# Kernel optimization log

Hardware: AMD Instinct MI355X
Metric: run time of the kernel (lower is better)

The kernel has to match this reference:

```python
import jax, jax.numpy as jnp
import numpy as np

K = 3  # per_pix_kernel


def conv2d(x, w, b, pad):
    y = jax.lax.conv_general_dilated(
        x, w, window_strides=(1, 1), padding=[(pad, pad), (pad, pad)],
        dimension_numbers=('NCHW', 'OIHW', 'NCHW'))
    return y + b[None, :, None, None]


def per_pix_apply(x, kmap):
    # x: [B,C,H,W]; kmap: [B,K*K,H,W] (tanh-activated per-pixel kernels)
    # out[b,c,h,w] = sum_j patch_j(x)[b,c,h,w] * kmap[b,j,h,w]
    B, C, H, W = x.shape
    p = K // 2
    xp = jnp.pad(x, ((0, 0), (0, 0), (p, p), (p, p)))
    patches = jnp.stack(
        [xp[:, :, di:di + H, dj:dj + W] for di in range(K) for dj in range(K)],
        axis=1)  # [B, K*K, C, H, W]
    return jnp.einsum('bjchw,bjhw->bchw', patches, kmap)


def setup_inputs() -> dict:
    key = jax.random.key(0)
    ks = jax.random.split(key, 7)
    B, C, H, W = 4, 64, 256, 256
    kk = K * K  # 9
    s = 0.05
    return {
        'feature': jax.random.normal(ks[0], (B, C, H, W), jnp.float32),
        'w_sharp': jax.random.normal(ks[1], (kk, C, 5, 5), jnp.float32) * s,
        'b_sharp': jnp.zeros((kk,), jnp.float32),
        'w_r1': jax.random.normal(ks[2], (kk, C, 3, 3), jnp.float32) * s,
        'b_r1': jnp.zeros((kk,), jnp.float32),
        'w_r2': jax.random.normal(ks[3], (kk, kk, 3, 3), jnp.float32) * s,
        'b_r2': jnp.zeros((kk,), jnp.float32),
    }


def reference(feature, w_sharp, b_sharp, w_r1, b_r1, w_r2, b_r2):
    # sharp_attention = local_conv: 5x5 conv -> tanh -> per-pixel dynamic filter
    att_kernels = jnp.tanh(conv2d(feature, w_sharp, b_sharp, pad=2))  # [B,9,H,W]
    attention_feature = per_pix_apply(feature, att_kernels)           # [B,C,H,W]
    # reblur_filer (ratio == 1): conv3x3 -> conv3x3 -> tanh
    d = feature - attention_feature
    r = conv2d(d, w_r1, b_r1, pad=1)
    r = conv2d(r, w_r2, b_r2, pad=1)
    reblur_filter = jnp.tanh(r)  # [B,9,H,W]
    return reblur_filter, attention_feature
```

## Files before the change

kernel.cpp:

```cpp
#include <hip/hip_runtime.h>

#define B_ 4
#define C_ 64
#define H_ 256
#define W_ 256
#define KK 9

typedef __attribute__((ext_vector_type(8))) short short8;
typedef __attribute__((ext_vector_type(4))) float float4_;

static __device__ __forceinline__ unsigned short f2bf(float f) {
    unsigned int u = __builtin_bit_cast(unsigned int, f);
    unsigned int r = (u + 0x7fffu + ((u >> 16) & 1u)) >> 16;
    return (unsigned short)r;
}
static __device__ __forceinline__ float bf2f(short s) {
    return __builtin_bit_cast(float, (unsigned int)((unsigned short)s) << 16);
}

__global__ __launch_bounds__(256) void nchw2nhwc(
    const float* __restrict__ x, unsigned short* __restrict__ xh)
{
    __shared__ unsigned short t[256 * 66];
    int row = blockIdx.x;
    int b = row >> 8;
    const float* src = x + ((size_t)b * 64) * 65536 + (size_t)(row & 255) * 256;
    int tid = threadIdx.x;

    #pragma unroll 4
    for (int c = 0; c < 64; ++c)
        t[tid * 66 + c] = f2bf(src[(size_t)c * 65536 + tid]);
    __syncthreads();

    unsigned short* dst = xh + (size_t)row * 256 * 64;
    #pragma unroll
    for (int it = 0; it < 8; ++it) {
        int idx = it * 256 + tid;
        int pix = idx >> 3, g = idx & 7;
        short8 v = *(const short8*)(&t[pix * 66 + g * 8]);
        *(short8*)(dst + (size_t)pix * 64 + g * 8) = v;
    }
}

__global__ __launch_bounds__(256) void wprep_all(
    const float* __restrict__ w5, const float* __restrict__ w3,
    unsigned short* __restrict__ wb, unsigned short* __restrict__ wb3)
{
    int i = blockIdx.x * 256 + threadIdx.x;
    if (i < 25600) {
        int tap = i >> 10;
        int q = (i >> 7) & 7;
        int n = (i >> 3) & 15;
        int e = i & 7;
        int c = q * 8 + e;
        int di = tap / 5, dj = tap % 5;
        float v = (n < KK) ? w5[((n * C_ + c) * 5 + di) * 5 + dj] : 0.f;
        wb[i] = f2bf(v);
    } else if (i < 34816) {
        int k = i - 25600;
        int tap = k >> 10;
        int q = (k >> 7) & 7;
        int n = (k >> 3) & 15;
        int e = k & 7;
        int c = q * 8 + e;
        int di = tap / 3, dj = tap % 3;
        float v = (n < KK) ? w3[((n * C_ + c) * 3 + di) * 3 + dj] : 0.f;
        wb3[k] = f2bf(v);
    }
}

__global__ __launch_bounds__(256) void conv5_mfma(
    const unsigned short* __restrict__ xh,
    const unsigned short* __restrict__ wb,
    const float* __restrict__ bias,
    unsigned short* __restrict__ att)
{
    __shared__ unsigned short xs[20 * 20 * 64];

    int tid = threadIdx.x;
    int bx = blockIdx.x & 15;
    int by = (blockIdx.x >> 4) & 15;
    int b  = blockIdx.x >> 8;
    int h0 = by * 16, w0 = bx * 16;

    for (int q = tid; q < 400 * 8; q += 256) {
        int p = q & 7;
        int pix = q >> 3;
        int py = pix / 20, px = pix % 20;
        int gy = h0 + py - 2, gx = w0 + px - 2;
        short8 v = (short8)0;
        if (gy >= 0 && gy < H_ && gx >= 0 && gx < W_)
            v = *(const short8*)(xh + ((size_t)((b * 256 + gy) * 256 + gx) * 64 + p * 8));
        *(short8*)(&xs[(pix << 6) + ((p ^ (pix & 7)) << 3)]) = v;
    }
    __syncthreads();

    int lane = tid & 63;
    int wid  = tid >> 6;
    int m16  = lane & 15;
    int lq   = lane >> 4;

    float4_ acc[4];
    float bj = (m16 < KK) ? bias[m16] : 0.f;
    #pragma unroll
    for (int r = 0; r < 4; ++r) acc[r] = (float4_){bj, bj, bj, bj};

    #pragma unroll
    for (int dj = 0; dj < 5; ++dj) {
        short8 bfr[5][2];
        #pragma unroll
        for (int di = 0; di < 5; ++di) {
            int tap = di * 5 + dj;
            bfr[di][0] = *(const short8*)(wb + (((tap * 8 + lq) * 16 + m16) * 8));
            bfr[di][1] = *(const short8*)(wb + (((tap * 8 + 4 + lq) * 16 + m16) * 8));
        }
        int px = m16 + dj;
        #pragma unroll
        for (int s = 0; s < 8; ++s) {
            int pix = (wid * 4 + s) * 20 + px;
            int c0 = lq ^ (pix & 7);
            short8 a0 = *(const short8*)(&xs[(pix << 6) + (c0 << 3)]);
            short8 a1 = *(const short8*)(&xs[(pix << 6) + ((c0 ^ 4) << 3)]);
            #pragma unroll
            for (int di = 0; di < 5; ++di) {
                int r = s - di;
                if (r < 0 || r > 3) continue;
                acc[r] = __builtin_amdgcn_mfma_f32_16x16x32_bf16(a0, bfr[di][0], acc[r], 0, 0, 0);
                acc[r] = __builtin_amdgcn_mfma_f32_16x16x32_bf16(a1, bfr[di][1], acc[r], 0, 0, 0);
            }
        }
    }

    if (m16 < KK) {
        #pragma unroll
        for (int r = 0; r < 4; ++r) {
            int py = h0 + wid * 4 + r;
            #pragma unroll
            for (int reg = 0; reg < 4; ++reg) {
                int px = w0 + lq * 4 + reg;
                att[((b * KK + m16) << 16) | (py << 8) | px] = f2bf(tanhf(acc[r][reg]));
            }
        }
    }
}

__global__ __launch_bounds__(256) void perpix_nhwc(
    const unsigned short* __restrict__ xh, const unsigned short* __restrict__ att,
    float* __restrict__ attf, unsigned short* __restrict__ dh)
{
    int t = blockIdx.x * 256 + threadIdx.x;
    int g = t & 7;
    int pix = t >> 3;
    int b = pix >> 16;
    int hw = pix & 65535;
    int h = hw >> 8, w = hw & 255;

    float a[KK];
    #pragma unroll
    for (int j = 0; j < KK; ++j)
        a[j] = bf2f(att[((b * KK + j) << 16) | hw]);

    float s[8] = {0, 0, 0, 0, 0, 0, 0, 0};
    float xc[8] = {0, 0, 0, 0, 0, 0, 0, 0};
    #pragma unroll
    for (int di = 0; di < 3; ++di) {
        int y = h + di - 1;
        #pragma unroll
        for (int dj = 0; dj < 3; ++dj) {
            int xq = w + dj - 1;
            if (y < 0 || y >= H_ || xq < 0 || xq >= W_) continue;
            short8 v = *(const short8*)(xh + ((size_t)((b << 16) | (y << 8) | xq) * 64 + g * 8));
            float aj = a[di * 3 + dj];
            #pragma unroll
            for (int i = 0; i < 8; ++i) {
                float xv = bf2f(v[i]);
                s[i] += xv * aj;
                if (di == 1 && dj == 1) xc[i] = xv;
            }
        }
    }

    #pragma unroll
    for (int i = 0; i < 8; ++i)
        attf[((size_t)(b * C_ + g * 8 + i) << 16) | hw] = s[i];

    short8 dv;
    #pragma unroll
    for (int i = 0; i < 8; ++i) dv[i] = (short)f2bf(xc[i] - s[i]);
    *(short8*)(dh + (size_t)pix * 64 + g * 8) = dv;
}

__global__ __launch_bounds__(256) void conv3_mfma(
    const unsigned short* __restrict__ dh,
    const unsigned short* __restrict__ wb3,
    const float* __restrict__ bias,
    unsigned short* __restrict__ r1h)
{
    __shared__ unsigned short xs[18 * 18 * 64];

    int tid = threadIdx.x;
    int bx = blockIdx.x & 15;
    int by = (blockIdx.x >> 4) & 15;
    int b  = blockIdx.x >> 8;
    int h0 = by * 16, w0 = bx * 16;

    for (int q = tid; q < 324 * 8; q += 256) {
        int p = q & 7;
        int pix = q >> 3;
        int py = pix / 18, px = pix % 18;
        int gy = h0 + py - 1, gx = w0 + px - 1;
        short8 v = (short8)0;
        if (gy >= 0 && gy < H_ && gx >= 0 && gx < W_)
            v = *(const short8*)(dh + ((size_t)((b * 256 + gy) * 256 + gx) * 64 + p * 8));
        *(short8*)(&xs[(pix << 6) + ((p ^ (pix & 7)) << 3)]) = v;
    }
    __syncthreads();

    int lane = tid & 63;
    int wid  = tid >> 6;
    int m16  = lane & 15;
    int lq   = lane >> 4;

    float4_ acc[4];
    float bj = (m16 < KK) ? bias[m16] : 0.f;
    #pragma unroll
    for (int r = 0; r < 4; ++r) acc[r] = (float4_){bj, bj, bj, bj};

    #pragma unroll
    for (int dj = 0; dj < 3; ++dj) {
        short8 bfr[3][2];
        #pragma unroll
        for (int di = 0; di < 3; ++di) {
            int tap = di * 3 + dj;
            bfr[di][0] = *(const short8*)(wb3 + (((tap * 8 + lq) * 16 + m16) * 8));
            bfr[di][1] = *(const short8*)(wb3 + (((tap * 8 + 4 + lq) * 16 + m16) * 8));
        }
        int px = m16 + dj;
        #pragma unroll
        for (int s = 0; s < 6; ++s) {
            int pix = (wid * 4 + s) * 18 + px;
            int c0 = lq ^ (pix & 7);
            short8 a0 = *(const short8*)(&xs[(pix << 6) + (c0 << 3)]);
            short8 a1 = *(const short8*)(&xs[(pix << 6) + ((c0 ^ 4) << 3)]);
            #pragma unroll
            for (int di = 0; di < 3; ++di) {
                int r = s - di;
                if (r < 0 || r > 3) continue;
                acc[r] = __builtin_amdgcn_mfma_f32_16x16x32_bf16(a0, bfr[di][0], acc[r], 0, 0, 0);
                acc[r] = __builtin_amdgcn_mfma_f32_16x16x32_bf16(a1, bfr[di][1], acc[r], 0, 0, 0);
            }
        }
    }

    if (m16 < KK) {
        #pragma unroll
        for (int r = 0; r < 4; ++r) {
            int py = h0 + wid * 4 + r;
            #pragma unroll
            for (int reg = 0; reg < 4; ++reg) {
                int px = w0 + lq * 4 + reg;
                r1h[((b * KK + m16) << 16) | (py << 8) | px] = f2bf(acc[r][reg]);
            }
        }
    }
}

__global__ __launch_bounds__(256) void conv3_tanh9(
    const unsigned short* __restrict__ r1h, const float* __restrict__ w,
    const float* __restrict__ bias, float* __restrict__ out)
{
    const int TW = 32, TH = 8, PW = 34, PH = 10;
    __shared__ float lds[KK][PH][PW];

    int tid = threadIdx.x;
    int tx = tid & 31, ty = tid >> 5;
    int bw = blockIdx.x & 7;
    int bh = (blockIdx.x >> 3) & 31;
    int b  = blockIdx.x >> 8;
    int h0 = bh * TH, w0 = bw * TW;

    for (int idx = tid; idx < KK * PH * PW; idx += 256) {
        int px = idx % PW;
        int py = (idx / PW) % PH;
        int ch = idx / (PW * PH);
        int gy = h0 + py - 1, gx = w0 + px - 1;
        float v = 0.f;
        if (gy >= 0 && gy < H_ && gx >= 0 && gx < W_)
            v = bf2f(r1h[((b * KK + ch) << 16) | (gy << 8) | gx]);
        lds[ch][py][px] = v;
    }
    __syncthreads();

    float acc[KK];
    #pragma unroll
    for (int j = 0; j < KK; ++j) acc[j] = bias[j];

    for (int cin = 0; cin < KK; ++cin) {
        #pragma unroll
        for (int di = 0; di < 3; ++di) {
            #pragma unroll
            for (int dj = 0; dj < 3; ++dj) {
                float xv = lds[cin][ty + di][tx + dj];
                #pragma unroll
                for (int j = 0; j < KK; ++j)
                    acc[j] += xv * w[((j * KK + cin) * 3 + di) * 3 + dj];
            }
        }
    }

    int h = h0 + ty, wq = w0 + tx;
    #pragma unroll
    for (int j = 0; j < KK; ++j)
        out[((b * KK + j) << 16) | (h << 8) | wq] = tanhf(acc[j]);
}

extern "C" void kernel_launch(void* const* d_in, const int* in_sizes, int n_in,
                              void* d_out, int out_size, void* d_ws, size_t ws_size,
                              hipStream_t stream) {
    const float* feature = (const float*)d_in[0];
    const float* w_sharp = (const float*)d_in[1];
    const float* b_sharp = (const float*)d_in[2];
    const float* w_r1    = (const float*)d_in[3];
    const float* b_r1    = (const float*)d_in[4];
    const float* w_r2    = (const float*)d_in[5];
    const float* b_r2    = (const float*)d_in[6];

    float* out_reblur = (float*)d_out;
    float* out_attf   = out_reblur + (size_t)B_ * KK * H_ * W_;

    char* ws = (char*)d_ws;
    unsigned short* xh   = (unsigned short*)ws;
    unsigned short* dh   = (unsigned short*)(ws + 33554432);
    unsigned short* wb   = (unsigned short*)(ws + 67108864);
    unsigned short* wb3  = (unsigned short*)(ws + 67174400);
    unsigned short* att  = (unsigned short*)(ws + 67207168);
    unsigned short* r1h  = att;

    nchw2nhwc<<<1024, 256, 0, stream>>>(feature, xh);
    wprep_all<<<136, 256, 0, stream>>>(w_sharp, w_r1, wb, wb3);
    conv5_mfma<<<1024, 256, 0, stream>>>(xh, wb, b_sharp, att);
    perpix_nhwc<<<8192, 256, 0, stream>>>(xh, att, out_attf, dh);
    conv3_mfma<<<1024, 256, 0, stream>>>(dh, wb3, b_r1, r1h);
    conv3_tanh9<<<1024, 256, 0, stream>>>(r1h, w_r2, b_r2, out_reblur);
}
```

Baseline: 123.6 us.

## Fuse per-pixel filter into first 3x3 conv and use direct global-to-LDS loads

The per-pixel dynamic filter is folded into the first 3x3 conv kernel. It stages a 20x20 NHWC tile of the input in LDS, computes the difference tensor for the 18x18 halo in registers, and writes it back to LDS before the MFMA conv. This drops the round trip of the bf16 difference tensor through global memory and removes one launch, at the cost of recomputing the halo pixels. Interior tiles also stage through global_load_lds direct-to-LDS loads instead of register round trips. The new kernel uses more registers (11 short8 held across the phase) and a larger LDS footprint.

Measured after the change: 118.0 us. 1.05x faster.

```diff
diff --git a/kernel.cpp b/kernel.cpp
--- a/kernel.cpp
+++ b/kernel.cpp
@@ -16,6 +16,11 @@
 }
 static __device__ __forceinline__ float bf2f(short s) {
     return __builtin_bit_cast(float, (unsigned int)((unsigned short)s) << 16);
+}
+static __device__ __forceinline__ void gld16(const unsigned short* gp, unsigned short* lbase) {
+    __builtin_amdgcn_global_load_lds(
+        (const __attribute__((address_space(1))) unsigned int*)gp,
+        (__attribute__((address_space(3))) unsigned int*)lbase, 16, 0, 0);
 }
 
 __global__ __launch_bounds__(256) void nchw2nhwc(
@@ -69,6 +74,35 @@
     }
 }
 
+static __device__ __forceinline__ void stage20(
+    const unsigned short* __restrict__ xh, unsigned short* xs,
+    int b, int h0, int w0, bool interior, int tid)
+{
+    if (interior) {
+        int lane = tid & 63, wid = tid >> 6;
+        int p = (lane & 7) ^ ((lane >> 3) & 7);
+        int sub = lane >> 3;
+        for (int it = wid; it < 50; it += 4) {
+            int pix = it * 8 + sub;
+            int py = pix / 20, px = pix % 20;
+            int gy = h0 + py - 2, gx = w0 + px - 2;
+            const unsigned short* g = xh + ((size_t)((b * 256 + gy) * 256 + gx) * 64 + p * 8);
+            gld16(g, &xs[it * 512]);
+        }
+    } else {
+        for (int q = tid; q < 400 * 8; q += 256) {
+            int p = q & 7;
+            int pix = q >> 3;
+            int py = pix / 20, px = pix % 20;
+            int gy = h0 + py - 2, gx = w0 + px - 2;
+            short8 v = (short8)0;
+            if (gy >= 0 && gy < H_ && gx >= 0 && gx < W_)
+                v = *(const short8*)(xh + ((size_t)((b * 256 + gy) * 256 + gx) * 64 + p * 8));
+            *(short8*)(&xs[(pix << 6) + ((p ^ (pix & 7)) << 3)]) = v;
+        }
+    }
+}
+
 __global__ __launch_bounds__(256) void conv5_mfma(
     const unsigned short* __restrict__ xh,
     const unsigned short* __restrict__ wb,
@@ -82,17 +116,9 @@
     int by = (blockIdx.x >> 4) & 15;
     int b  = blockIdx.x >> 8;
     int h0 = by * 16, w0 = bx * 16;
-
-    for (int q = tid; q < 400 * 8; q += 256) {
-        int p = q & 7;
-        int pix = q >> 3;
-        int py = pix / 20, px = pix % 20;
-        int gy = h0 + py - 2, gx = w0 + px - 2;
-        short8 v = (short8)0;
-        if (gy >= 0 && gy < H_ && gx >= 0 && gx < W_)
-            v = *(const short8*)(xh + ((size_t)((b * 256 + gy) * 256 + gx) * 64 + p * 8));
-        *(short8*)(&xs[(pix << 6) + ((p ^ (pix & 7)) << 3)]) = v;
-    }
+    bool interior = (bx >= 1 && bx <= 14 && by >= 1 && by <= 14);
+
+    stage20(xh, xs, b, h0, w0, interior, tid);
     __syncthreads();
 
     int lane = tid & 63;
@@ -144,75 +170,83 @@
     }
 }
 
-__global__ __launch_bounds__(256) void perpix_nhwc(
-    const unsigned short* __restrict__ xh, const unsigned short* __restrict__ att,
-    float* __restrict__ attf, unsigned short* __restrict__ dh)
-{
-    int t = blockIdx.x * 256 + threadIdx.x;
-    int g = t & 7;
-    int pix = t >> 3;
-    int b = pix >> 16;
-    int hw = pix & 65535;
-    int h = hw >> 8, w = hw & 255;
-
-    float a[KK];
-    #pragma unroll
-    for (int j = 0; j < KK; ++j)
-        a[j] = bf2f(att[((b * KK + j) << 16) | hw]);
-
-    float s[8] = {0, 0, 0, 0, 0, 0, 0, 0};
-    float xc[8] = {0, 0, 0, 0, 0, 0, 0, 0};
-    #pragma unroll
-    for (int di = 0; di < 3; ++di) {
-        int y = h + di - 1;
-        #pragma unroll
-        for (int dj = 0; dj < 3; ++dj) {
-            int xq = w + dj - 1;
-            if (y < 0 || y >= H_ || xq < 0 || xq >= W_) continue;
-            short8 v = *(const short8*)(xh + ((size_t)((b << 16) | (y << 8) | xq) * 64 + g * 8));
-            float aj = a[di * 3 + dj];
-            #pragma unroll
-            for (int i = 0; i < 8; ++i) {
-                float xv = bf2f(v[i]);
-                s[i] += xv * aj;
-                if (di == 1 && dj == 1) xc[i] = xv;
-            }
-        }
-    }
-
-    #pragma unroll
-    for (int i = 0; i < 8; ++i)
-        attf[((size_t)(b * C_ + g * 8 + i) << 16) | hw] = s[i];
-
-    short8 dv;
-    #pragma unroll
-    for (int i = 0; i < 8; ++i) dv[i] = (short)f2bf(xc[i] - s[i]);
-    *(short8*)(dh + (size_t)pix * 64 + g * 8) = dv;
-}
-
-__global__ __launch_bounds__(256) void conv3_mfma(
-    const unsigned short* __restrict__ dh,
+__global__ __launch_bounds__(256) void conv3_fused(
+    const unsigned short* __restrict__ xh,
+    const unsigned short* __restrict__ att,
     const unsigned short* __restrict__ wb3,
     const float* __restrict__ bias,
+    float* __restrict__ attf,
     unsigned short* __restrict__ r1h)
 {
-    __shared__ unsigned short xs[18 * 18 * 64];
+    __shared__ unsigned short xs[20 * 20 * 64];
 
     int tid = threadIdx.x;
     int bx = blockIdx.x & 15;
     int by = (blockIdx.x >> 4) & 15;
     int b  = blockIdx.x >> 8;
     int h0 = by * 16, w0 = bx * 16;
-
-    for (int q = tid; q < 324 * 8; q += 256) {
-        int p = q & 7;
-        int pix = q >> 3;
-        int py = pix / 18, px = pix % 18;
-        int gy = h0 + py - 1, gx = w0 + px - 1;
-        short8 v = (short8)0;
-        if (gy >= 0 && gy < H_ && gx >= 0 && gx < W_)
-            v = *(const short8*)(dh + ((size_t)((b * 256 + gy) * 256 + gx) * 64 + p * 8));
-        *(short8*)(&xs[(pix << 6) + ((p ^ (pix & 7)) << 3)]) = v;
+    bool interior = (bx >= 1 && bx <= 14 && by >= 1 && by <= 14);
+
+    stage20(xh, xs, b, h0, w0, interior, tid);
+    __syncthreads();
+
+    short8 dreg[11];
+    #pragma unroll
+    for (int it = 0; it < 11; ++it) {
+        dreg[it] = (short8)0;
+        int idx = it * 256 + tid;
+        if (idx < 2592) {
+            int g = idx & 7;
+            int pix = idx >> 3;
+            int py = pix / 18, px = pix % 18;
+            int gy = h0 + py - 1, gx = w0 + px - 1;
+            if (gy >= 0 && gy < H_ && gx >= 0 && gx < W_) {
+                int hw = (gy << 8) | gx;
+                float a[KK];
+                #pragma unroll
+                for (int j = 0; j < KK; ++j)
+                    a[j] = bf2f(att[((b * KK + j) << 16) | hw]);
+
+                float s[8] = {0, 0, 0, 0, 0, 0, 0, 0};
+                float xc[8];
+                #pragma unroll
+                for (int di = 0; di < 3; ++di) {
+                    #pragma unroll
+                    for (int dj = 0; dj < 3; ++dj) {
+                        int pix20 = (py + di) * 20 + (px + dj);
+                        int c = g ^ (pix20 & 7);
+                        short8 v = *(const short8*)(&xs[(pix20 << 6) + (c << 3)]);
+                        float aj = a[di * 3 + dj];
+                        #pragma unroll
+                        for (int i = 0; i < 8; ++i) {
+                            float xv = bf2f(v[i]);
+                            s[i] += xv * aj;
+                            if (di == 1 && dj == 1) xc[i] = xv;
+                        }
+                    }
+                }
+                if (py >= 1 && py <= 16 && px >= 1 && px <= 16) {
+                    #pragma unroll
+                    for (int i = 0; i < 8; ++i)
+                        attf[((b * C_ + g * 8 + i) << 16) | hw] = s[i];
+                }
+                short8 dv;
+                #pragma unroll
+                for (int i = 0; i < 8; ++i) dv[i] = (short)f2bf(xc[i] - s[i]);
+                dreg[it] = dv;
+            }
+        }
+    }
+    __syncthreads();
+
+    #pragma unroll
+    for (int it = 0; it < 11; ++it) {
+        int idx = it * 256 + tid;
+        if (idx < 2592) {
+            int g = idx & 7;
+            int pix = idx >> 3;
+            *(short8*)(&xs[(pix << 6) + ((g ^ (pix & 7)) << 3)]) = dreg[it];
+        }
     }
     __syncthreads();
 
@@ -330,16 +364,14 @@
 
     char* ws = (char*)d_ws;
     unsigned short* xh   = (unsigned short*)ws;
-    unsigned short* dh   = (unsigned short*)(ws + 33554432);
-    unsigned short* wb   = (unsigned short*)(ws + 67108864);
-    unsigned short* wb3  = (unsigned short*)(ws + 67174400);
-    unsigned short* att  = (unsigned short*)(ws + 67207168);
-    unsigned short* r1h  = att;
+    unsigned short* wb   = (unsigned short*)(ws + 33554432);
+    unsigned short* wb3  = (unsigned short*)(ws + 33619968);
+    unsigned short* att  = (unsigned short*)(ws + 33652736);
+    unsigned short* r1h  = (unsigned short*)(ws + 38371328);
 
     nchw2nhwc<<<1024, 256, 0, stream>>>(feature, xh);
     wprep_all<<<136, 256, 0, stream>>>(w_sharp, w_r1, wb, wb3);
     conv5_mfma<<<1024, 256, 0, stream>>>(xh, wb, b_sharp, att);
-    perpix_nhwc<<<8192, 256, 0, stream>>>(xh, att, out_attf, dh);
-    conv3_mfma<<<1024, 256, 0, stream>>>(dh, wb3, b_r1, r1h);
+    conv3_fused<<<1024, 256, 0, stream>>>(xh, att, wb3, b_r1, out_attf, r1h);
     conv3_tanh9<<<1024, 256, 0, stream>>>(r1h, w_r2, b_r2, out_reblur);
 }
```

## Fuse per-pixel dynamic filter into conv5 kernel and use direct global-to-LDS loads

Applied to the files above, without the earlier changes.

The 5x5 attention conv and the per-pixel 3x3 dynamic filter are merged into one kernel. The tanh kernel maps stay in shared memory, and the filter reads the already-staged 20x20 input tile from LDS instead of re-reading xh from global memory. This drops one launch, the att round trip through global memory, and the 9x global gathers. Separately, interior tiles in the conv5 and conv3 kernels now stage their inputs with global_load_lds 16-byte transfers, while border tiles keep the guarded path. The risks are more LDS per block, which may lower occupancy, and a per-thread 8-iteration filter loop over 256 pixels that could lengthen the tail of each block.

Result: faster. 106.2 us (-14.0%).

```diff
diff --git a/kernel.cpp b/kernel.cpp
--- a/kernel.cpp
+++ b/kernel.cpp
@@ -16,6 +16,11 @@
 }
 static __device__ __forceinline__ float bf2f(short s) {
     return __builtin_bit_cast(float, (unsigned int)((unsigned short)s) << 16);
+}
+static __device__ __forceinline__ void gld16(const unsigned short* gp, unsigned short* lbase) {
+    __builtin_amdgcn_global_load_lds(
+        (const __attribute__((address_space(1))) unsigned int*)gp,
+        (__attribute__((address_space(3))) unsigned int*)lbase, 16, 0, 0);
 }
 
 __global__ __launch_bounds__(256) void nchw2nhwc(
@@ -69,29 +74,45 @@
     }
 }
 
-__global__ __launch_bounds__(256) void conv5_mfma(
+__global__ __launch_bounds__(256) void conv5_perpix(
     const unsigned short* __restrict__ xh,
     const unsigned short* __restrict__ wb,
     const float* __restrict__ bias,
-    unsigned short* __restrict__ att)
-{
-    __shared__ unsigned short xs[20 * 20 * 64];
+    float* __restrict__ attf,
+    unsigned short* __restrict__ dh)
+{
+    __shared__ __align__(16) unsigned short xs[20 * 20 * 64];
+    __shared__ unsigned short att_s[256 * 9];
 
     int tid = threadIdx.x;
     int bx = blockIdx.x & 15;
     int by = (blockIdx.x >> 4) & 15;
     int b  = blockIdx.x >> 8;
     int h0 = by * 16, w0 = bx * 16;
-
-    for (int q = tid; q < 400 * 8; q += 256) {
-        int p = q & 7;
-        int pix = q >> 3;
-        int py = pix / 20, px = pix % 20;
-        int gy = h0 + py - 2, gx = w0 + px - 2;
-        short8 v = (short8)0;
-        if (gy >= 0 && gy < H_ && gx >= 0 && gx < W_)
-            v = *(const short8*)(xh + ((size_t)((b * 256 + gy) * 256 + gx) * 64 + p * 8));
-        *(short8*)(&xs[(pix << 6) + ((p ^ (pix & 7)) << 3)]) = v;
+    bool interior = (bx >= 1 && bx <= 14 && by >= 1 && by <= 14);
+
+    if (interior) {
+        int lane = tid & 63, wid = tid >> 6;
+        int p = (lane & 7) ^ ((lane >> 3) & 7);
+        int sub = lane >> 3;
+        for (int it = wid; it < 50; it += 4) {
+            int pix = it * 8 + sub;
+            int py = pix / 20, px = pix % 20;
+            int gy = h0 + py - 2, gx = w0 + px - 2;
+            const unsigned short* g = xh + ((size_t)((b * 256 + gy) * 256 + gx) * 64 + p * 8);
+            gld16(g, &xs[it * 512]);
+        }
+    } else {
+        for (int q = tid; q < 400 * 8; q += 256) {
+            int p = q & 7;
+            int pix = q >> 3;
+            int py = pix / 20, px = pix % 20;
+            int gy = h0 + py - 2, gx = w0 + px - 2;
+            short8 v = (short8)0;
+            if (gy >= 0 && gy < H_ && gx >= 0 && gx < W_)
+                v = *(const short8*)(xh + ((size_t)((b * 256 + gy) * 256 + gx) * 64 + p * 8));
+            *(short8*)(&xs[(pix << 6) + ((p ^ (pix & 7)) << 3)]) = v;
+        }
     }
     __syncthreads();
 
@@ -134,60 +155,55 @@
     if (m16 < KK) {
         #pragma unroll
         for (int r = 0; r < 4; ++r) {
-            int py = h0 + wid * 4 + r;
             #pragma unroll
             for (int reg = 0; reg < 4; ++reg) {
-                int px = w0 + lq * 4 + reg;
-                att[((b * KK + m16) << 16) | (py << 8) | px] = f2bf(tanhf(acc[r][reg]));
-            }
-        }
-    }
-}
-
-__global__ __launch_bounds__(256) void perpix_nhwc(
-    const unsigned short* __restrict__ xh, const unsigned short* __restrict__ att,
-    float* __restrict__ attf, unsigned short* __restrict__ dh)
-{
-    int t = blockIdx.x * 256 + threadIdx.x;
-    int g = t & 7;
-    int pix = t >> 3;
-    int b = pix >> 16;
-    int hw = pix & 65535;
-    int h = hw >> 8, w = hw & 255;
-
-    float a[KK];
-    #pragma unroll
-    for (int j = 0; j < KK; ++j)
-        a[j] = bf2f(att[((b * KK + j) << 16) | hw]);
-
-    float s[8] = {0, 0, 0, 0, 0, 0, 0, 0};
-    float xc[8] = {0, 0, 0, 0, 0, 0, 0, 0};
-    #pragma unroll
-    for (int di = 0; di < 3; ++di) {
-        int y = h + di - 1;
-        #pragma unroll
-        for (int dj = 0; dj < 3; ++dj) {
-            int xq = w + dj - 1;
-            if (y < 0 || y >= H_ || xq < 0 || xq >= W_) continue;
-            short8 v = *(const short8*)(xh + ((size_t)((b << 16) | (y << 8) | xq) * 64 + g * 8));
-            float aj = a[di * 3 + dj];
-            #pragma unroll
-            for (int i = 0; i < 8; ++i) {
-                float xv = bf2f(v[i]);
-                s[i] += xv * aj;
-                if (di == 1 && dj == 1) xc[i] = xv;
-            }
-        }
-    }
-
-    #pragma unroll
-    for (int i = 0; i < 8; ++i)
-        attf[((size_t)(b * C_ + g * 8 + i) << 16) | hw] = s[i];
-
-    short8 dv;
-    #pragma unroll
-    for (int i = 0; i < 8; ++i) dv[i] = (short)f2bf(xc[i] - s[i]);
-    *(short8*)(dh + (size_t)pix * 64 + g * 8) = dv;
+                int pl = (wid * 4 + r) * 16 + lq * 4 + reg;
+                att_s[pl * 9 + m16] = f2bf(tanhf(acc[r][reg]));
+            }
+        }
+    }
+    __syncthreads();
+
+    #pragma unroll
+    for (int it = 0; it < 8; ++it) {
+        int idx = it * 256 + tid;
+        int g = idx & 7;
+        int pl = idx >> 3;
+        int py = pl >> 4, px = pl & 15;
+        int hw = ((h0 + py) << 8) | (w0 + px);
+
+        float a[KK];
+        #pragma unroll
+        for (int j = 0; j < KK; ++j) a[j] = bf2f(att_s[pl * 9 + j]);
+
+        float s[8] = {0, 0, 0, 0, 0, 0, 0, 0};
+        float xc[8] = {0, 0, 0, 0, 0, 0, 0, 0};
+        #pragma unroll
+        for (int di = 0; di < 3; ++di) {
+            #pragma unroll
+            for (int dj = 0; dj < 3; ++dj) {
+                int tp = (py + 1 + di) * 20 + (px + 1 + dj);
+                int c = g ^ (tp & 7);
+                short8 v = *(const short8*)(&xs[(tp << 6) + (c << 3)]);
+                float aj = a[di * 3 + dj];
+                #pragma unroll
+                for (int i = 0; i < 8; ++i) {
+                    float xv = bf2f(v[i]);
+                    s[i] += xv * aj;
+                    if (di == 1 && dj == 1) xc[i] = xv;
+                }
+            }
+        }
+
+        #pragma unroll
+        for (int i = 0; i < 8; ++i)
+            attf[((b * C_ + g * 8 + i) << 16) | hw] = s[i];
+
+        short8 dv;
+        #pragma unroll
+        for (int i = 0; i < 8; ++i) dv[i] = (short)f2bf(xc[i] - s[i]);
+        *(short8*)(dh + ((size_t)((b << 16) | hw) * 64 + g * 8)) = dv;
+    }
 }
 
 __global__ __launch_bounds__(256) void conv3_mfma(
@@ -196,23 +212,37 @@
     const float* __restrict__ bias,
     unsigned short* __restrict__ r1h)
 {
-    __shared__ unsigned short xs[18 * 18 * 64];
+    __shared__ __align__(16) unsigned short xs[328 * 64];
 
     int tid = threadIdx.x;
     int bx = blockIdx.x & 15;
     int by = (blockIdx.x >> 4) & 15;
     int b  = blockIdx.x >> 8;
     int h0 = by * 16, w0 = bx * 16;
-
-    for (int q = tid; q < 324 * 8; q += 256) {
-        int p = q & 7;
-        int pix = q >> 3;
-        int py = pix / 18, px = pix % 18;
-        int gy = h0 + py - 1, gx = w0 + px - 1;
-        short8 v = (short8)0;
-        if (gy >= 0 && gy < H_ && gx >= 0 && gx < W_)
-            v = *(const short8*)(dh + ((size_t)((b * 256 + gy) * 256 + gx) * 64 + p * 8));
-        *(short8*)(&xs[(pix << 6) + ((p ^ (pix & 7)) << 3)]) = v;
+    bool interior = (bx >= 1 && bx <= 14 && by >= 1 && by <= 14);
+
+    if (interior) {
+        int lane = tid & 63, wid = tid >> 6;
+        int p = (lane & 7) ^ ((lane >> 3) & 7);
+        int sub = lane >> 3;
+        for (int it = wid; it < 41; it += 4) {
+            int pix = it * 8 + sub;
+            int py = pix / 18, px = pix - py * 18;
+            int gy = h0 + py - 1, gx = w0 + px - 1;
+            const unsigned short* g = dh + ((size_t)((b * 256 + gy) * 256 + gx) * 64 + p * 8);
+            gld16(g, &xs[it * 512]);
+        }
+    } else {
+        for (int q = tid; q < 324 * 8; q += 256) {
+            int p = q & 7;
+            int pix = q >> 3;
+            int py = pix / 18, px = pix - py * 18;
+            int gy = h0 + py - 1, gx = w0 + px - 1;
+            short8 v = (short8)0;
+            if (gy >= 0 && gy < H_ && gx >= 0 && gx < W_)
+                v = *(const short8*)(dh + ((size_t)((b * 256 + gy) * 256 + gx) * 64 + p * 8));
+            *(short8*)(&xs[(pix << 6) + ((p ^ (pix & 7)) << 3)]) = v;
+        }
     }
     __syncthreads();
 
@@ -333,13 +363,11 @@
     unsigned short* dh   = (unsigned short*)(ws + 33554432);
     unsigned short* wb   = (unsigned short*)(ws + 67108864);
     unsigned short* wb3  = (unsigned short*)(ws + 67174400);
-    unsigned short* att  = (unsigned short*)(ws + 67207168);
-    unsigned short* r1h  = att;
+    unsigned short* r1h  = (unsigned short*)(ws + 67207168);
 
     nchw2nhwc<<<1024, 256, 0, stream>>>(feature, xh);
     wprep_all<<<136, 256, 0, stream>>>(w_sharp, w_r1, wb, wb3);
-    conv5_mfma<<<1024, 256, 0, stream>>>(xh, wb, b_sharp, att);
-    perpix_nhwc<<<8192, 256, 0, stream>>>(xh, att, out_attf, dh);
+    conv5_perpix<<<1024, 256, 0, stream>>>(xh, wb, b_sharp, out_attf, dh);
     conv3_mfma<<<1024, 256, 0, stream>>>(dh, wb3, b_r1, r1h);
     conv3_tanh9<<<1024, 256, 0, stream>>>(r1h, w_r2, b_r2, out_reblur);
 }
```
